# Performance work log

Measured on AMD Instinct MI355X. Metric: run time of the kernel, lower is better.

The kernel has to match this reference:

```python
import jax, jax.numpy as jnp
import numpy as np

# Detector / Siddon constants (from init_kwargs)
H, W = 200, 200
DELX, DELY = 1.5, 1.5
NXV, NYV, NZV = 256, 256, 256  # voxel counts
EPS = 1e-8


def setup_inputs() -> dict:
    key = jax.random.key(0)
    kvol, = jax.random.split(key, 1)
    volume = jax.random.uniform(kvol, (NXV, NYV, NZV), dtype=jnp.float32)  # CT intensities
    spacing = jnp.ones((3,), jnp.float32)                                  # 1mm isotropic
    sdr = jnp.array([300.0], jnp.float32)                                  # source-to-detector radius
    rotations = jnp.array([[0.5, -0.2, 0.3]], jnp.float32)                 # theta, phi, gamma
    translations = jnp.array([[128.0, 128.0, 128.0]], jnp.float32)         # volume center (bx,by,bz)
    return {"volume": volume, "spacing": spacing, "sdr": sdr,
            "rotations": rotations, "translations": translations}


def _rotation_matrix(rotations):
    # R = Rz(theta) @ Ry(phi) @ Rx(gamma), batched
    theta, phi, gamma = rotations[:, 0], rotations[:, 1], rotations[:, 2]
    ct, st = jnp.cos(theta), jnp.sin(theta)
    cp, sp = jnp.cos(phi), jnp.sin(phi)
    cg, sg = jnp.cos(gamma), jnp.sin(gamma)
    z = jnp.zeros_like(theta)
    o = jnp.ones_like(theta)
    Rz = jnp.stack([ct, -st, z, st, ct, z, z, z, o], -1).reshape(-1, 3, 3)
    Ry = jnp.stack([cp, z, sp, z, o, z, -sp, z, cp], -1).reshape(-1, 3, 3)
    Rx = jnp.stack([o, z, z, z, cg, -sg, z, sg, cg], -1).reshape(-1, 3, 3)
    return Rz @ Ry @ Rx


def _make_xrays(sdr, rotations, translations):
    # Detector.make_xrays: source on column 0 of sdr*R, detector center opposite,
    # detector plane spanned by unit columns 1 and 2.
    R = _rotation_matrix(rotations)                 # (b,3,3), orthonormal columns
    source = sdr[:, None] * R[..., 0]               # (b,3)
    center = -source
    basis = jnp.stack([R[..., 1], R[..., 2]], 1)    # (b,2,3)
    source = source + translations
    center = center + translations
    t = (jnp.arange(-(H // 2), H // 2, dtype=jnp.float32) + 1.0) * DELX
    s = (jnp.arange(-(W // 2), W // 2, dtype=jnp.float32) + 1.0) * DELY
    coefs = jnp.stack(jnp.meshgrid(t, s, indexing="ij"), -1).reshape(-1, 2)  # (H*W,2) == cartesian_prod(t,s)
    target = jnp.einsum("bcd,nc->bnd", basis, coefs) + center[:, None, :]    # (b,n,3)
    return source[:, None, :], target               # (b,1,3), (b,n,3)


def reference(volume, spacing, sdr, rotations, translations):
    source, target = _make_xrays(sdr, rotations, translations)
    vol = jnp.flip(volume, 0)                       # Siddon flips axis 0
    nx, ny, nz = vol.shape
    sdd = target - source + EPS                     # (b,n,3) ray directions

    # Alphas at every axis-aligned plane intersection: P = (nx+1)+(ny+1)+(nz+1)
    alphas = jnp.concatenate(
        [(jnp.arange(n + 1, dtype=jnp.float32) * spacing[i] - source[..., i:i + 1]) / sdd[..., i:i + 1]
         for i, n in enumerate((nx, ny, nz))], axis=-1)          # (b,n,P)

    # Entry/exit alphas of the volume bounding box
    extent = jnp.asarray([nx, ny, nz], jnp.float32) * spacing
    a0 = (0.0 - source) / sdd
    a1 = (extent - source) / sdd
    amin = jnp.max(jnp.minimum(a0, a1), -1, keepdims=True)       # (b,n,1)
    amax = jnp.min(jnp.maximum(a0, a1), -1, keepdims=True)

    # Out-of-range alphas -> sentinel amax (sorts to the end, contributes zero step;
    # equivalent to the original's NaN + nansum handling)
    valid = (alphas >= amin) & (alphas <= amax)
    alphas = jnp.sort(jnp.where(valid, alphas, amax), axis=-1)

    mid = 0.5 * (alphas[..., :-1] + alphas[..., 1:])             # (b,n,P-1)
    step = jnp.diff(alphas, axis=-1)

    # Midpoint positions -> voxel indices (trunc, clamped in-bounds)
    xyz = source[:, :, None, :] + mid[..., None] * sdd[:, :, None, :]  # (b,n,P-1,3)
    idx = jnp.trunc(xyz / spacing).astype(jnp.int32)
    ix = jnp.clip(idx[..., 0], 0, nx - 1)
    iy = jnp.clip(idx[..., 1], 0, ny - 1)
    iz = jnp.clip(idx[..., 2], 0, nz - 1)
    voxels = vol[ix, iy, iz]                                     # gather, (b,n,P-1)

    drr = jnp.sum(voxels * step, -1) * jnp.linalg.norm(sdd, axis=-1)
    return drr.reshape(-1, H, W)
```

## Files before the change

### kernel.cpp

```cpp
#include <hip/hip_runtime.h>

#define H_ 200
#define W_ 200
#define DELX_ 1.5f
#define DELY_ 1.5f
#define NXV_ 256
#define NYV_ 256
#define NZV_ 256
#define EPS_ 1e-8f
#define NSEG 16
#define SEGS_PER_BLK 8
#define TILE_R 4
#define TILE_C 16
#define TROWS (H_ / TILE_R)
#define TCOLS ((W_ + TILE_C - 1) / TILE_C)
#define TILES_PER_IMG (TROWS * TCOLS)
#define G_ 8
#define MAXG 10

__device__ __forceinline__ float alpha_mul(float k, float sp, float src, float inv_sdd) {
    return (k * sp - src) * inv_sdd;
}

#define MARCH(OFF, STP)                                                       \
    _Pragma("unroll")                                                         \
    for (int u = 0; u < G_; ++u) {                                            \
        float an = fminf(axv, fminf(ayv, azv));                               \
        bool ok = (an <= aend);                                               \
        STP[u] = ok ? (an - a_cur) : 0.0f;                                    \
        OFF[u] = off_cur;                                                     \
        a_cur = an;                                                           \
        bool upd = (an < aend);                                               \
        bool cx = (axv == an), cy = (ayv == an), cz = (azv == an);            \
        kx = cx ? kx + dkx : kx;                                              \
        ky = cy ? ky + dky : ky;                                              \
        kz = cz ? kz + dkz : kz;                                              \
        off_cur += ((cx && upd) ? doffx : 0)                                  \
                 + ((cy && upd) ? doffy : 0)                                  \
                 + ((cz && upd) ? doffz : 0);                                 \
        axv = alpha_mul(kx, spx, sx, inv_dx);   \
        ayv = alpha_mul(ky, spy, sy, inv_dy);                                 \
        azv = alpha_mul(kz, spz, sz, inv_dz);                                 \
    }

__global__ void __launch_bounds__(512, 6)
drr_partial(const float* __restrict__ vol,
            const float* __restrict__ spacing,
            const float* __restrict__ sdr,
            const float* __restrict__ rot,
            const float* __restrict__ trans,
            float* __restrict__ partials,
            int npix) {
    const int t = threadIdx.x;
    const int pixLocal = t & 63;
    const int half = blockIdx.x & 1;
    const int seg = (t >> 6) + (half << 3);
    const int tileBlk = blockIdx.x >> 1;

    const int b    = tileBlk / TILES_PER_IMG;
    const int rem  = tileBlk % TILES_PER_IMG;
    const int ty   = rem / TCOLS;
    const int tx   = rem % TCOLS;
    const int i = ty * TILE_R + (pixLocal >> 4);
    const int j = tx * TILE_C + (pixLocal & 15);

    const float theta = rot[b * 3 + 0], phi = rot[b * 3 + 1], gamma = rot[b * 3 + 2];
    const float ct = cosf(theta), st = sinf(theta);
    const float cp = cosf(phi),   sp = sinf(phi);
    const float cg = cosf(gamma), sg = sinf(gamma);
    const float r00 = ct * cp,                r10 = st * cp,                r20 = -sp;
    const float r01 = ct * sp * sg - st * cg, r11 = st * sp * sg + ct * cg, r21 = cp * sg;
    const float r02 = ct * sp * cg + st * sg, r12 = st * sp * cg - ct * sg, r22 = cp * cg;

    const float sd = sdr[b];
    const float tx_ = trans[b * 3 + 0], ty_ = trans[b * 3 + 1], tz_ = trans[b * 3 + 2];
    const float sx = sd * r00 + tx_, sy = sd * r10 + ty_, sz = sd * r20 + tz_;
    const float cxx = -sd * r00 + tx_, cyy = -sd * r10 + ty_, czz = -sd * r20 + tz_;

    const float tco = ((float)(i - H_ / 2) + 1.0f) * DELX_;
    const float sco = ((float)(j - W_ / 2) + 1.0f) * DELY_;
    const float gx = r01 * tco + r02 * sco + cxx;
    const float gy = r11 * tco + r12 * sco + cyy;
    const float gz = r21 * tco + r22 * sco + czz;

    const float dx = gx - sx + EPS_;
    const float dy = gy - sy + EPS_;
    const float dz = gz - sz + EPS_;

    const float spx = spacing[0], spy = spacing[1], spz = spacing[2];
    const float inv_spx = 1.0f / spx, inv_spy = 1.0f / spy, inv_spz = 1.0f / spz;
    const float inv_dx = 1.0f / dx, inv_dy = 1.0f / dy, inv_dz = 1.0f / dz;

    const float a0x = alpha_mul(0.f, spx, sx, inv_dx), a1x = alpha_mul((float)NXV_, spx, sx, inv_dx);
    const float a0y = alpha_mul(0.f, spy, sy, inv_dy), a1y = alpha_mul((float)NYV_, spy, sy, inv_dy);
    const float a0z = alpha_mul(0.f, spz, sz, inv_dz), a1z = alpha_mul((float)NZV_, spz, sz, inv_dz);

    const float amin = fmaxf(fmaxf(fminf(a0x, a1x), fminf(a0y, a1y)), fminf(a0z, a1z));
    const float amax = fminf(fminf(fmaxf(a0x, a1x), fmaxf(a0y, a1y)), fmaxf(a0z, a1z));

    const float norm = sqrtf(dx * dx + dy * dy + dz * dz);

    const float klo = (float)(seg * (NXV_ / NSEG));
    const float khi = (float)((seg + 1) * (NXV_ / NSEG));
    const float aA = alpha_mul(klo, spx, sx, inv_dx);
    const float aB = alpha_mul(khi, spx, sx, inv_dx);
    const float lo = fminf(aA, aB), hi = fmaxf(aA, aB);

    const float start = fmaxf(amin, lo);
    const float aend  = fminf(amax, hi);

    float acc = 0.0f;
    if (start < aend) {
        float kx, ky, kz, axv, ayv, azv, dkx, dky, dkz;
        {
            float kf = (start * dx + sx) * inv_spx;
            if (dx > 0.f) { dkx = 1.f;  kx = floorf(kf) + 1.f; }
            else          { dkx = -1.f; kx = ceilf(kf) - 1.f; }
            axv = alpha_mul(kx, spx, sx, inv_dx);
        }
        {
            float kf = (start * dy + sy) * inv_spy;
            if (dy > 0.f) { dky = 1.f;  ky = floorf(kf) + 1.f; }
            else          { dky = -1.f; ky = ceilf(kf) - 1.f; }
            ayv = alpha_mul(ky, spy, sy, inv_dy);
        }
        {
            float kf = (start * dz + sz) * inv_spz;
            if (dz > 0.f) { dkz = 1.f;  kz = floorf(kf) + 1.f; }
            else          { dkz = -1.f; kz = ceilf(kf) - 1.f; }
            azv = alpha_mul(kz, spz, sz, inv_dz);
        }

        int off_cur;
        {
            float an0 = fminf(axv, fminf(ayv, azv));
            float midv = 0.5f * (start + an0);
            int ix = (int)((sx + midv * dx) * inv_spx);
            int iy = (int)((sy + midv * dy) * inv_spy);
            int iz = (int)((sz + midv * dz) * inv_spz);
            ix = min(max(ix, 0), NXV_ - 1);
            iy = min(max(iy, 0), NYV_ - 1);
            iz = min(max(iz, 0), NZV_ - 1);
            off_cur = ((NXV_ - 1 - ix) * NYV_ + iy) * NZV_ + iz;
        }
        const int doffx = (dkx > 0.f) ? -(NYV_ * NZV_) : (NYV_ * NZV_);
        const int doffy = (dky > 0.f) ? NZV_ : -NZV_;
        const int doffz = (dkz > 0.f) ? 1 : -1;

        float a_cur = start;
        int   offA[G_], offB[G_];
        float stpA[G_], stpB[G_], v[G_];

        MARCH(offA, stpA);
        #pragma unroll 1
        for (int g = 0; g < MAXG; g += 2) {
            #pragma unroll
            for (int u = 0; u < G_; ++u) v[u] = vol[offA[u]];
            const bool moreA = !__all(a_cur > aend);
            if (moreA) { MARCH(offB, stpB); }
            #pragma unroll
            for (int u = 0; u < G_; ++u) acc += v[u] * stpA[u];
            if (!moreA) break;

            #pragma unroll
            for (int u = 0; u < G_; ++u) v[u] = vol[offB[u]];
            const bool moreB = !__all(a_cur > aend);
            if (moreB) { MARCH(offA, stpA); }
            #pragma unroll
            for (int u = 0; u < G_; ++u) acc += v[u] * stpB[u];
            if (!moreB) break;
        }
    }
    float result = acc * norm;

    __shared__ float red[SEGS_PER_BLK * 64];
    red[t] = result;
    __syncthreads();
    if (t < 64) {
        const int ii = ty * TILE_R + (t >> 4);
        const int jj = tx * TILE_C + (t & 15);
        if (jj < W_) {
            const int opix = b * (H_ * W_) + ii * W_ + jj;
            float s = 0.0f;
            #pragma unroll
            for (int k = 0; k < SEGS_PER_BLK; k++) s += red[t + k * 64];
            partials[(size_t)half * npix + opix] = s;
        }
    }
}

__global__ void __launch_bounds__(256)
drr_combine(const float* __restrict__ partials, float* __restrict__ out, int npix) {
    int pix = blockIdx.x * blockDim.x + threadIdx.x;
    if (pix >= npix) return;
    out[pix] = partials[pix] + partials[(size_t)npix + pix];
}

extern "C" void kernel_launch(void* const* d_in, const int* in_sizes, int n_in,
                              void* d_out, int out_size, void* d_ws, size_t ws_size,
                              hipStream_t stream) {
    const float* vol     = (const float*)d_in[0];
    const float* spacing = (const float*)d_in[1];
    const float* sdr     = (const float*)d_in[2];
    const float* rot     = (const float*)d_in[3];
    const float* trans   = (const float*)d_in[4];
    float* out = (float*)d_out;

    const int B = in_sizes[2];
    const int npix = B * H_ * W_;
    float* partials = (float*)d_ws;

    const int nblocks = B * TILES_PER_IMG * 2;
    drr_partial<<<nblocks, 64 * SEGS_PER_BLK, 0, stream>>>(vol, spacing, sdr, rot, trans, partials, npix);
    drr_combine<<<(npix + 255) / 256, 256, 0, stream>>>(partials, out, npix);
}
```

Before: 129.6 us.

## Fuse partial and combine kernels by looping two segments per thread

Each thread now marches two x-slabs sequentially instead of launching twice as many blocks, and the block sums all 16 segments in shared memory to write the output directly. This removes the second combine kernel launch and the partials round trip through global memory. It also drops the double-buffered march/load software pipelining in favour of a simple march-then-load loop. The cost is half as many blocks, so less parallelism and latency hiding, with each thread's work serialized across two segments.

New measurement: 121.2 us. 6.5% less time.

```diff
diff --git a/kernel.cpp b/kernel.cpp
--- a/kernel.cpp
+++ b/kernel.cpp
@@ -9,7 +9,7 @@
 #define NZV_ 256
 #define EPS_ 1e-8f
 #define NSEG 16
-#define SEGS_PER_BLK 8
+#define SEGS_PER_THR 2
 #define TILE_R 4
 #define TILE_C 16
 #define TROWS (H_ / TILE_R)
@@ -44,21 +44,18 @@
     }
 
 __global__ void __launch_bounds__(512, 6)
-drr_partial(const float* __restrict__ vol,
-            const float* __restrict__ spacing,
-            const float* __restrict__ sdr,
-            const float* __restrict__ rot,
-            const float* __restrict__ trans,
-            float* __restrict__ partials,
-            int npix) {
+drr_tile(const float* __restrict__ vol,
+         const float* __restrict__ spacing,
+         const float* __restrict__ sdr,
+         const float* __restrict__ rot,
+         const float* __restrict__ trans,
+         float* __restrict__ out) {
     const int t = threadIdx.x;
     const int pixLocal = t & 63;
-    const int half = blockIdx.x & 1;
-    const int seg = (t >> 6) + (half << 3);
-    const int tileBlk = blockIdx.x >> 1;
+    const int segBase = t >> 6;
 
-    const int b    = tileBlk / TILES_PER_IMG;
-    const int rem  = tileBlk % TILES_PER_IMG;
+    const int b    = blockIdx.x / TILES_PER_IMG;
+    const int rem  = blockIdx.x % TILES_PER_IMG;
     const int ty   = rem / TCOLS;
     const int tx   = rem % TCOLS;
     const int i = ty * TILE_R + (pixLocal >> 4);
@@ -100,100 +97,89 @@
 
     const float norm = sqrtf(dx * dx + dy * dy + dz * dz);
 
-    const float klo = (float)(seg * (NXV_ / NSEG));
-    const float khi = (float)((seg + 1) * (NXV_ / NSEG));
-    const float aA = alpha_mul(klo, spx, sx, inv_dx);
-    const float aB = alpha_mul(khi, spx, sx, inv_dx);
-    const float lo = fminf(aA, aB), hi = fmaxf(aA, aB);
+    const int doffy0 = NZV_, doffz0 = 1;
 
-    const float start = fmaxf(amin, lo);
-    const float aend  = fminf(amax, hi);
+    __shared__ float red[NSEG * 64];
 
-    float acc = 0.0f;
-    if (start < aend) {
-        float kx, ky, kz, axv, ayv, azv, dkx, dky, dkz;
-        {
-            float kf = (start * dx + sx) * inv_spx;
-            if (dx > 0.f) { dkx = 1.f;  kx = floorf(kf) + 1.f; }
-            else          { dkx = -1.f; kx = ceilf(kf) - 1.f; }
-            axv = alpha_mul(kx, spx, sx, inv_dx);
+    #pragma unroll 1
+    for (int s2 = 0; s2 < SEGS_PER_THR; ++s2) {
+        const int seg = segBase + (s2 << 3);
+
+        const float klo = (float)(seg * (NXV_ / NSEG));
+        const float khi = (float)((seg + 1) * (NXV_ / NSEG));
+        const float aA = alpha_mul(klo, spx, sx, inv_dx);
+        const float aB = alpha_mul(khi, spx, sx, inv_dx);
+        const float start = fmaxf(amin, fminf(aA, aB));
+        const float aend  = fminf(amax, fmaxf(aA, aB));
+
+        float acc = 0.0f;
+        if (start < aend) {
+            float kx, ky, kz, axv, ayv, azv, dkx, dky, dkz;
+            {
+                float kf = (start * dx + sx) * inv_spx;
+                if (dx > 0.f) { dkx = 1.f;  kx = floorf(kf) + 1.f; }
+                else          { dkx = -1.f; kx = ceilf(kf) - 1.f; }
+                axv = alpha_mul(kx, spx, sx, inv_dx);
+            }
+            {
+                float kf = (start * dy + sy) * inv_spy;
+                if (dy > 0.f) { dky = 1.f;  ky = floorf(kf) + 1.f; }
+                else          { dky = -1.f; ky = ceilf(kf) - 1.f; }
+                ayv = alpha_mul(ky, spy, sy, inv_dy);
+            }
+            {
+                float kf = (start * dz + sz) * inv_spz;
+                if (dz > 0.f) { dkz = 1.f;  kz = floorf(kf) + 1.f; }
+                else          { dkz = -1.f; kz = ceilf(kf) - 1.f; }
+                azv = alpha_mul(kz, spz, sz, inv_dz);
+            }
+
+            int off_cur;
+            {
+                float an0 = fminf(axv, fminf(ayv, azv));
+                float midv = 0.5f * (start + an0);
+                int ix = (int)((sx + midv * dx) * inv_spx);
+                int iy = (int)((sy + midv * dy) * inv_spy);
+                int iz = (int)((sz + midv * dz) * inv_spz);
+                ix = min(max(ix, 0), NXV_ - 1);
+                iy = min(max(iy, 0), NYV_ - 1);
+                iz = min(max(iz, 0), NZV_ - 1);
+                off_cur = ((NXV_ - 1 - ix) * NYV_ + iy) * NZV_ + iz;
+            }
+            const int doffx = (dkx > 0.f) ? -(NYV_ * NZV_) : (NYV_ * NZV_);
+            const int doffy = (dky > 0.f) ? doffy0 : -doffy0;
+            const int doffz = (dkz > 0.f) ? doffz0 : -doffz0;
+
+            float a_cur = start;
+            int   off[G_];
+            float stp[G_], v[G_];
+
+            #pragma unroll 1
+            for (int g = 0; g < MAXG; ++g) {
+                MARCH(off, stp);
+                #pragma unroll
+                for (int u = 0; u < G_; ++u) v[u] = vol[off[u]];
+                #pragma unroll
+                for (int u = 0; u < G_; ++u) acc += v[u] * stp[u];
+                if (__all(a_cur > aend)) break;
+            }
         }
-        {
-            float kf = (start * dy + sy) * inv_spy;
-            if (dy > 0.f) { dky = 1.f;  ky = floorf(kf) + 1.f; }
-            else          { dky = -1.f; ky = ceilf(kf) - 1.f; }
-            ayv = alpha_mul(ky, spy, sy, inv_dy);
-        }
-        {
-            float kf = (start * dz + sz) * inv_spz;
-            if (dz > 0.f) { dkz = 1.f;  kz = floorf(kf) + 1.f; }
-            else          { dkz = -1.f; kz = ceilf(kf) - 1.f; }
-            azv = alpha_mul(kz, spz, sz, inv_dz);
-        }
+        red[(s2 << 9) + t] = acc * norm;
+    }
 
-        int off_cur;
-        {
-            float an0 = fminf(axv, fminf(ayv, azv));
-            float midv = 0.5f * (start + an0);
-            int ix = (int)((sx + midv * dx) * inv_spx);
-            int iy = (int)((sy + midv * dy) * inv_spy);
-            int iz = (int)((sz + midv * dz) * inv_spz);
-            ix = min(max(ix, 0), NXV_ - 1);
-            iy = min(max(iy, 0), NYV_ - 1);
-            iz = min(max(iz, 0), NZV_ - 1);
-            off_cur = ((NXV_ - 1 - ix) * NYV_ + iy) * NZV_ + iz;
-        }
-        const int doffx = (dkx > 0.f) ? -(NYV_ * NZV_) : (NYV_ * NZV_);
-        const int doffy = (dky > 0.f) ? NZV_ : -NZV_;
-        const int doffz = (dkz > 0.f) ? 1 : -1;
-
-        float a_cur = start;
-        int   offA[G_], offB[G_];
-        float stpA[G_], stpB[G_], v[G_];
-
-        MARCH(offA, stpA);
-        #pragma unroll 1
-        for (int g = 0; g < MAXG; g += 2) {
-            #pragma unroll
-            for (int u = 0; u < G_; ++u) v[u] = vol[offA[u]];
-            const bool moreA = !__all(a_cur > aend);
-            if (moreA) { MARCH(offB, stpB); }
-            #pragma unroll
-            for (int u = 0; u < G_; ++u) acc += v[u] * stpA[u];
-            if (!moreA) break;
-
-            #pragma unroll
-            for (int u = 0; u < G_; ++u) v[u] = vol[offB[u]];
-            const bool moreB = !__all(a_cur > aend);
-            if (moreB) { MARCH(offA, stpA); }
-            #pragma unroll
-            for (int u = 0; u < G_; ++u) acc += v[u] * stpB[u];
-            if (!moreB) break;
-        }
-    }
-    float result = acc * norm;
-
-    __shared__ float red[SEGS_PER_BLK * 64];
-    red[t] = result;
     __syncthreads();
     if (t < 64) {
         const int ii = ty * TILE_R + (t >> 4);
         const int jj = tx * TILE_C + (t & 15);
         if (jj < W_) {
-            const int opix = b * (H_ * W_) + ii * W_ + jj;
-            float s = 0.0f;
+            float sLo = 0.0f, sHi = 0.0f;
             #pragma unroll
-            for (int k = 0; k < SEGS_PER_BLK; k++) s += red[t + k * 64];
-            partials[(size_t)half * npix + opix] = s;
+            for (int k = 0; k < 8; ++k) sLo += red[t + k * 64];
+            #pragma unroll
+            for (int k = 0; k < 8; ++k) sHi += red[512 + t + k * 64];
+            out[b * (H_ * W_) + ii * W_ + jj] = sLo + sHi;
         }
     }
-}
-
-__global__ void __launch_bounds__(256)
-drr_combine(const float* __restrict__ partials, float* __restrict__ out, int npix) {
-    int pix = blockIdx.x * blockDim.x + threadIdx.x;
-    if (pix >= npix) return;
-    out[pix] = partials[pix] + partials[(size_t)npix + pix];
 }
 
 extern "C" void kernel_launch(void* const* d_in, const int* in_sizes, int n_in,
@@ -207,10 +193,5 @@
     float* out = (float*)d_out;
 
     const int B = in_sizes[2];
-    const int npix = B * H_ * W_;
-    float* partials = (float*)d_ws;
-
-    const int nblocks = B * TILES_PER_IMG * 2;
-    drr_partial<<<nblocks, 64 * SEGS_PER_BLK, 0, stream>>>(vol, spacing, sdr, rot, trans, partials, npix);
-    drr_combine<<<(npix + 255) / 256, 256, 0, stream>>>(partials, out, npix);
+    drr_tile<<<B * TILES_PER_IMG, 512, 0, stream>>>(vol, spacing, sdr, rot, trans, out);
 }
```

## Issue voxel loads inside march loop and remap workgroups across XCDs

Applied to the files above, without the earlier changes.

The ray march now loads each voxel as soon as its offset is computed and folds the previous group's accumulation into the same unrolled loop, instead of storing offsets and loading them in a separate batch. The goal is to overlap gather latency with march arithmetic and to drop the offset arrays. It also remaps blockIdx so that consecutive logical workgroups land on the same XCD, and now splits segment halves by the first and second half of the grid, which should improve L2 locality. The cost is more live registers, since value and step buffers are double-buffered, and a different compiler schedule.

Result: slower. 167.4 us (+29.1%).

```diff
diff --git a/kernel.cpp b/kernel.cpp
--- a/kernel.cpp
+++ b/kernel.cpp
@@ -22,13 +22,13 @@
     return (k * sp - src) * inv_sdd;
 }
 
-#define MARCH(OFF, STP)                                                       \
+#define MARCH_ISSUE(VC, SC)                                                   \
     _Pragma("unroll")                                                         \
     for (int u = 0; u < G_; ++u) {                                            \
         float an = fminf(axv, fminf(ayv, azv));                               \
         bool ok = (an <= aend);                                               \
-        STP[u] = ok ? (an - a_cur) : 0.0f;                                    \
-        OFF[u] = off_cur;                                                     \
+        SC[u] = ok ? (an - a_cur) : 0.0f;                                     \
+        VC[u] = vol[off_cur];                 \
         a_cur = an;                                                           \
         bool upd = (an < aend);                                               \
         bool cx = (axv == an), cy = (ayv == an), cz = (azv == an);            \
@@ -43,6 +43,32 @@
         azv = alpha_mul(kz, spz, sz, inv_dz);                                 \
     }
 
+#define MARCH_ISSUE_CONSUME(VC, SC, VP, SP)                                   \
+    _Pragma("unroll")                                                         \
+    for (int u = 0; u < G_; ++u) {                                            \
+        acc += VP[u] * SP[u];               \
+        float an = fminf(axv, fminf(ayv, azv));                               \
+        bool ok = (an <= aend);                                               \
+        SC[u] = ok ? (an - a_cur) : 0.0f;                                     \
+        VC[u] = vol[off_cur];                                                 \
+        a_cur = an;                                                           \
+        bool upd = (an < aend);                                               \
+        bool cx = (axv == an), cy = (ayv == an), cz = (azv == an);            \
+        kx = cx ? kx + dkx : kx;                                              \
+        ky = cy ? ky + dky : ky;                                              \
+        kz = cz ? kz + dkz : kz;                                              \
+        off_cur += ((cx && upd) ? doffx : 0)                                  \
+                 + ((cy && upd) ? doffy : 0)                                  \
+                 + ((cz && upd) ? doffz : 0);                                 \
+        axv = alpha_mul(kx, spx, sx, inv_dx);                                 \
+        ayv = alpha_mul(ky, spy, sy, inv_dy);                                 \
+        azv = alpha_mul(kz, spz, sz, inv_dz);                                 \
+    }
+
+#define CONSUME(VP, SP)                                                       \
+    _Pragma("unroll")                                                         \
+    for (int u = 0; u < G_; ++u) { acc += VP[u] * SP[u]; }
+
 __global__ void __launch_bounds__(512, 6)
 drr_partial(const float* __restrict__ vol,
             const float* __restrict__ spacing,
@@ -51,11 +77,19 @@
             const float* __restrict__ trans,
             float* __restrict__ partials,
             int npix) {
+    const int nwg = gridDim.x;
+    const int q8 = nwg >> 3, r8 = nwg & 7;
+    const int xcd = blockIdx.x & 7;
+    const int sub = blockIdx.x >> 3;
+    const int wg = (xcd < r8 ? xcd * (q8 + 1) : r8 * (q8 + 1) + (xcd - r8) * q8) + sub;
+
+    const int ntiles = nwg >> 1;
+    const int half    = (wg < ntiles) ? 0 : 1;
+    const int tileBlk = wg - half * ntiles;
+
     const int t = threadIdx.x;
     const int pixLocal = t & 63;
-    const int half = blockIdx.x & 1;
     const int seg = (t >> 6) + (half << 3);
-    const int tileBlk = blockIdx.x >> 1;
 
     const int b    = tileBlk / TILES_PER_IMG;
     const int rem  = tileBlk % TILES_PER_IMG;
@@ -104,10 +138,8 @@
     const float khi = (float)((seg + 1) * (NXV_ / NSEG));
     const float aA = alpha_mul(klo, spx, sx, inv_dx);
     const float aB = alpha_mul(khi, spx, sx, inv_dx);
-    const float lo = fminf(aA, aB), hi = fmaxf(aA, aB);
-
-    const float start = fmaxf(amin, lo);
-    const float aend  = fminf(amax, hi);
+    const float start = fmaxf(amin, fminf(aA, aB));
+    const float aend  = fminf(amax, fmaxf(aA, aB));
 
     float acc = 0.0f;
     if (start < aend) {
@@ -148,27 +180,16 @@
         const int doffz = (dkz > 0.f) ? 1 : -1;
 
         float a_cur = start;
-        int   offA[G_], offB[G_];
-        float stpA[G_], stpB[G_], v[G_];
-
-        MARCH(offA, stpA);
+        float vA[G_], sA[G_], vB[G_], sB[G_];
+
+        MARCH_ISSUE(vA, sA);
+        int g = 1;
         #pragma unroll 1
-        for (int g = 0; g < MAXG; g += 2) {
-            #pragma unroll
-            for (int u = 0; u < G_; ++u) v[u] = vol[offA[u]];
-            const bool moreA = !__all(a_cur > aend);
-            if (moreA) { MARCH(offB, stpB); }
-            #pragma unroll
-            for (int u = 0; u < G_; ++u) acc += v[u] * stpA[u];
-            if (!moreA) break;
-
-            #pragma unroll
-            for (int u = 0; u < G_; ++u) v[u] = vol[offB[u]];
-            const bool moreB = !__all(a_cur > aend);
-            if (moreB) { MARCH(offA, stpA); }
-            #pragma unroll
-            for (int u = 0; u < G_; ++u) acc += v[u] * stpB[u];
-            if (!moreB) break;
+        while (true) {
+            if (__all(a_cur > aend) || g >= MAXG) { CONSUME(vA, sA); break; }
+            MARCH_ISSUE_CONSUME(vB, sB, vA, sA); ++g;
+            if (__all(a_cur > aend) || g >= MAXG) { CONSUME(vB, sB); break; }
+            MARCH_ISSUE_CONSUME(vA, sA, vB, sB); ++g;
         }
     }
     float result = acc * norm;
```
